# Performance work log

Hardware: AMD Instinct MI355X
Metric: run time of the kernel (lower is better)

## Reference

```python
import jax, jax.numpy as jnp
import numpy as np

N = 100000   # nodes (batched graph)
E = 1600000  # edges
G = 2048     # molecules in the batch
D_IN = 128
D_H = 128
MLP_H = 512


def setup_inputs() -> dict:
    key = jax.random.key(0)
    ks = jax.random.split(key, 20)

    def w(k, i, o):
        return (jax.random.normal(k, (i, o), jnp.float32) / np.sqrt(i)).astype(jnp.float32)

    feats = jax.random.normal(ks[0], (N, D_IN), jnp.float32)
    src = jax.random.randint(ks[1], (E,), 0, N)
    dst = jax.random.randint(ks[2], (E,), 0, N)
    graph_ids = jnp.sort(jax.random.randint(ks[3], (N,), 0, G))

    return {
        "feats": feats, "src": src, "dst": dst, "graph_ids": graph_ids,
        # 3 GraphConv layers
        "W0": w(ks[4], D_IN, D_H), "b0": jnp.zeros((D_H,), jnp.float32),
        "W1": w(ks[5], D_H, D_H),  "b1": jnp.zeros((D_H,), jnp.float32),
        "W2": w(ks[6], D_H, D_H),  "b2": jnp.zeros((D_H,), jnp.float32),
        # MLP head: D_H -> 512 -> 256 -> 1
        "Wm0": w(ks[7], D_H, MLP_H),       "bm0": jnp.zeros((MLP_H,), jnp.float32),
        "Wm1": w(ks[8], MLP_H, MLP_H // 2), "bm1": jnp.zeros((MLP_H // 2,), jnp.float32),
        "Wm2": w(ks[9], MLP_H // 2, 1),     "bm2": jnp.zeros((1,), jnp.float32),
    }


def reference(feats, src, dst, graph_ids, W0, b0, W1, b1, W2, b2,
              Wm0, bm0, Wm1, bm1, Wm2, bm2):
    ones_e = jnp.ones((E,), jnp.float32)
    # DGL GraphConv norm='both': D_out^{-1/2} on src, D_in^{-1/2} on dst; deg clamped to 1
    deg_out = jnp.maximum(jax.ops.segment_sum(ones_e, src, num_segments=N), 1.0)
    deg_in = jnp.maximum(jax.ops.segment_sum(ones_e, dst, num_segments=N), 1.0)
    inv_src = jax.lax.rsqrt(deg_out)[:, None]
    inv_dst = jax.lax.rsqrt(deg_in)[:, None]

    def gcn_layer(h, W, b):
        h = h * inv_src                                   # [N, D]
        m = jax.ops.segment_sum(h[src], dst, num_segments=N)  # gather-scatter over edges
        m = m * inv_dst
        return jax.nn.relu(jnp.dot(m, W) + b)

    h = gcn_layer(feats, W0, b0)
    h = gcn_layer(h, W1, b1)
    h = gcn_layer(h, W2, b2)

    # AvgPooling per graph
    counts = jnp.maximum(jax.ops.segment_sum(jnp.ones((N,), jnp.float32), graph_ids, num_segments=G), 1.0)
    emb = jax.ops.segment_sum(h, graph_ids, num_segments=G) / counts[:, None]  # [G, D_H]

    # MLP head (dropout = identity in eval)
    x = jax.nn.relu(jnp.dot(emb, Wm0) + bm0)
    x = jax.nn.relu(jnp.dot(x, Wm1) + bm1)
    return jnp.dot(x, Wm2) + bm2  # [G, 1]
```

## Files before the change

### kernel.cpp

```cpp
#include <hip/hip_runtime.h>


static inline int ceil_div(int a, int b){ return (a + b - 1) / b; }

#define B1 256
#define NBMAX 1024
#define CHUNK_MAX 7168
#define WPREP_BLOCKS 192

typedef __bf16 bf16x8 __attribute__((ext_vector_type(8)));
typedef float  f32x4  __attribute__((ext_vector_type(4)));

static __device__ inline __bf16 bits_to_bf16(unsigned short u){
  union { unsigned short u; __bf16 b; } x; x.u = u; return x.b;
}
static __device__ inline unsigned short bf16_bits(__bf16 b){
  union { __bf16 b; unsigned short u; } x; x.b = b; return x.u;
}
static __device__ inline unsigned pack_split(float s){
  __bf16 h = (__bf16)s;
  __bf16 l = (__bf16)(s - (float)h);
  return ((unsigned)bf16_bits(h) << 16) | (unsigned)bf16_bits(l);
}

__global__ __launch_bounds__(256) void scatter_count_kernel(
    const int* __restrict__ src, const int* __restrict__ dst,
    unsigned* __restrict__ cntA, unsigned* __restrict__ cntB,
    unsigned* __restrict__ stagedA, unsigned char* __restrict__ stagedB,
    const float* __restrict__ W0, const float* __restrict__ W1,
    const float* __restrict__ W2, __bf16* __restrict__ Wsp,
    int E, int NB){
  if (blockIdx.x >= B1){
    int gidx = (blockIdx.x - B1)*256 + threadIdx.x;
    if (gidx < 3*128*128){
      int layer = gidx >> 14, idx = gidx & 16383;
      const float* W = layer == 0 ? W0 : (layer == 1 ? W1 : W2);
      int k = idx >> 7, n = idx & 127;
      float w = W[idx];
      __bf16 h = (__bf16)w;
      __bf16 l = (__bf16)(w - (float)h);
      Wsp[(size_t)layer*2*16384 + n*128 + k] = h;
      Wsp[(size_t)layer*2*16384 + 16384 + n*128 + k] = l;
    }
    return;
  }

  __shared__ unsigned la[NBMAX], lb[NBMAX];
  __shared__ unsigned tsum[256];
  __shared__ unsigned stA[CHUNK_MAX];
  __shared__ unsigned char stB[CHUNK_MAX];

  const int t = threadIdx.x;
  const int blk = blockIdx.x;
  const int chunk = (E + B1 - 1) / B1;
  const int e0 = blk * chunk, e1 = min(e0 + chunk, E);
  const int len = e1 - e0;
  const int strideB = (chunk + 3) & ~3;

  #pragma unroll
  for (int i = t; i < NBMAX; i += 256){ la[i] = 0u; lb[i] = 0u; }
  __syncthreads();
  for (int e = e0 + t; e < e1; e += 256){
    atomicAdd(&la[dst[e] >> 7], 1u);
    atomicAdd(&lb[src[e] >> 7], 1u);
  }
  __syncthreads();

  for (int job = 0; job < 2; job++){
    unsigned* lx = job ? lb : la;
    unsigned* cx = job ? cntB : cntA;
    int b4 = t*4;
    unsigned v0 = lx[b4], v1 = lx[b4+1], v2 = lx[b4+2], v3 = lx[b4+3];
    unsigned s = v0+v1+v2+v3;
    tsum[t] = s;
    __syncthreads();
    for (int off = 1; off < 256; off <<= 1){
      unsigned u = (t >= off) ? tsum[t-off] : 0u;
      __syncthreads();
      tsum[t] += u;
      __syncthreads();
    }
    unsigned run = tsum[t] - s;
    unsigned o0 = run, o1 = run+v0, o2 = run+v0+v1, o3 = run+v0+v1+v2;
    lx[b4] = o0; lx[b4+1] = o1; lx[b4+2] = o2; lx[b4+3] = o3;
    if (b4   < NB) cx[(size_t)blk*NB + b4  ] = o0;
    if (b4+1 < NB) cx[(size_t)blk*NB + b4+1] = o1;
    if (b4+2 < NB) cx[(size_t)blk*NB + b4+2] = o2;
    if (b4+3 < NB) cx[(size_t)blk*NB + b4+3] = o3;
    __syncthreads();
  }

  for (int e = e0 + t; e < e1; e += 256){
    int s = src[e], d = dst[e];
    unsigned pA = atomicAdd(&la[d >> 7], 1u);
    stA[pA] = ((unsigned)(d & 127) << 17) | (unsigned)s;
    unsigned pB = atomicAdd(&lb[s >> 7], 1u);
    stB[pB] = (unsigned char)(s & 127);
  }
  __syncthreads();

  for (int i = t; i < len; i += 256)
    stagedA[(size_t)blk*chunk + i] = stA[i];
  int w4 = (len + 3) >> 2;
  unsigned* gB = (unsigned*)(stagedB + (size_t)blk*strideB);
  for (int i = t; i < w4; i += 256)
    gB[i] = *(unsigned*)&stB[4*i];
}

__global__ void totals_kernel(const unsigned* __restrict__ cntA,
                              const unsigned* __restrict__ cntB,
                              unsigned* __restrict__ totals, int NB, int E){
  int b = blockIdx.x * 256 + threadIdx.x;
  if (b >= NB) return;
  const unsigned* cx = blockIdx.y ? cntB : cntA;
  const int chunk = (E + B1 - 1) / B1;
  unsigned run = 0;
  for (int blk = 0; blk < B1; blk++){
    int lenb = E - blk*chunk; if (lenb > chunk) lenb = chunk; if (lenb < 0) lenb = 0;
    unsigned cur = cx[(size_t)blk*NB + b];
    unsigned nxt = (b < NB-1) ? cx[(size_t)blk*NB + b + 1] : (unsigned)lenb;
    run += nxt - cur;
  }
  totals[(size_t)blockIdx.y*NB + b] = run;
}

__global__ void scan_base_kernel(const unsigned* __restrict__ totals,
                                 unsigned* __restrict__ baseA, unsigned* __restrict__ baseB,
                                 int NB, int E){
  __shared__ unsigned s[NBMAX];
  int t = threadIdx.x;
  for (int job = 0; job < 2; job++){
    unsigned* base = job ? baseB : baseA;
    unsigned x = (t < NB) ? totals[(size_t)job*NB + t] : 0u;
    s[t] = x;
    __syncthreads();
    for (int off = 1; off < NBMAX; off <<= 1){
      unsigned v = (t >= off) ? s[t - off] : 0u;
      __syncthreads();
      s[t] += v;
      __syncthreads();
    }
    if (t < NB) base[t] = s[t] - x;
    if (t == 0) base[NB] = (unsigned)E;
    __syncthreads();
  }
}

__global__ __launch_bounds__(256) void csr_finalize_kernel(
    const unsigned* __restrict__ stagedA, const unsigned char* __restrict__ stagedB,
    const unsigned* __restrict__ cntA, const unsigned* __restrict__ cntB,
    const unsigned* __restrict__ baseA,
    int* __restrict__ row_ptr, float* __restrict__ inv_dst, float* __restrict__ inv_src,
    int* __restrict__ col, int N, int E, int NB){
  __shared__ unsigned cnt[128];
  __shared__ unsigned scn[128];
  const int b = blockIdx.x, t = threadIdx.x;
  const int node0 = b << 7;
  const int nn = min(128, N - node0);
  const int chunk = (E + B1 - 1) / B1;
  const int strideB = (chunk + 3) & ~3;
  int lenb = E - t*chunk; if (lenb > chunk) lenb = chunk; if (lenb < 0) lenb = 0;

  const unsigned a0 = cntA[(size_t)t*NB + b];
  const unsigned a1 = (b < NB-1) ? cntA[(size_t)t*NB + b + 1] : (unsigned)lenb;
  const unsigned* segA = stagedA + (size_t)t*chunk;

  if (t < 128) cnt[t] = 0u;
  __syncthreads();
  for (unsigned i = a0; i < a1; i++)
    atomicAdd(&cnt[(segA[i] >> 17) & 127u], 1u);
  __syncthreads();
  unsigned mycnt = (t < 128) ? cnt[t] : 0u;
  if (t < 128) scn[t] = mycnt;
  __syncthreads();
  for (int off = 1; off < 128; off <<= 1){
    unsigned v = (t < 128 && t >= off) ? scn[t - off] : 0u;
    __syncthreads();
    if (t < 128) scn[t] += v;
    __syncthreads();
  }
  int e0 = (int)baseA[b];
  if (t < nn){
    unsigned excl = scn[t] - mycnt;
    row_ptr[node0 + t] = e0 + (int)excl;
    unsigned c = mycnt < 1u ? 1u : mycnt;
    inv_dst[node0 + t] = rsqrtf((float)c);
    cnt[t] = (unsigned)e0 + excl;
  }
  if (b == NB - 1 && t == 0) row_ptr[N] = E;
  __syncthreads();
  for (unsigned i = a0; i < a1; i++){
    unsigned v = segA[i];
    unsigned p = atomicAdd(&cnt[(v >> 17) & 127u], 1u);
    col[p] = (int)(v & 0x1FFFFu);
  }
  __syncthreads();
  if (t < 128) cnt[t] = 0u;
  __syncthreads();
  const unsigned b0o = cntB[(size_t)t*NB + b];
  const unsigned b1o = (b < NB-1) ? cntB[(size_t)t*NB + b + 1] : (unsigned)lenb;
  const unsigned char* segB = stagedB + (size_t)t*strideB;
  for (unsigned i = b0o; i < b1o; i++)
    atomicAdd(&cnt[segB[i]], 1u);
  __syncthreads();
  if (t < nn){
    unsigned c = cnt[t] < 1u ? 1u : cnt[t];
    inv_src[node0 + t] = rsqrtf((float)c);
  }
}

template<bool SC>
__global__ __launch_bounds__(256) void csr_agg_kernel(
    const int* __restrict__ row_ptr, const int* __restrict__ col,
    const float* __restrict__ hs, const float* __restrict__ scale,
    const float* __restrict__ inv_dst, unsigned* __restrict__ aggp, int N){
  int node = (int)((blockIdx.x*256u + threadIdx.x) >> 5);
  int lane = threadIdx.x & 31;
  if (node >= N) return;
  int r0 = row_ptr[node];
  int r1 = row_ptr[node+1];
  float4 a0 = make_float4(0.f,0.f,0.f,0.f);
  float4 a1 = make_float4(0.f,0.f,0.f,0.f);
  float4 a2 = make_float4(0.f,0.f,0.f,0.f);
  float4 a3 = make_float4(0.f,0.f,0.f,0.f);
  int e = r0;
  for (; e + 3 < r1; e += 4){
    int s0 = col[e], s1 = col[e+1], s2 = col[e+2], s3 = col[e+3];
    float4 v0 = ((const float4*)(hs + (size_t)s0*128))[lane];
    float4 v1 = ((const float4*)(hs + (size_t)s1*128))[lane];
    float4 v2 = ((const float4*)(hs + (size_t)s2*128))[lane];
    float4 v3 = ((const float4*)(hs + (size_t)s3*128))[lane];
    if (SC){
      float c0 = scale[s0], c1 = scale[s1], c2 = scale[s2], c3 = scale[s3];
      v0.x*=c0; v0.y*=c0; v0.z*=c0; v0.w*=c0;
      v1.x*=c1; v1.y*=c1; v1.z*=c1; v1.w*=c1;
      v2.x*=c2; v2.y*=c2; v2.z*=c2; v2.w*=c2;
      v3.x*=c3; v3.y*=c3; v3.z*=c3; v3.w*=c3;
    }
    a0.x += v0.x; a0.y += v0.y; a0.z += v0.z; a0.w += v0.w;
    a1.x += v1.x; a1.y += v1.y; a1.z += v1.z; a1.w += v1.w;
    a2.x += v2.x; a2.y += v2.y; a2.z += v2.z; a2.w += v2.w;
    a3.x += v3.x; a3.y += v3.y; a3.z += v3.z; a3.w += v3.w;
  }
  for (; e < r1; e++){
    int s0 = col[e];
    float4 v0 = ((const float4*)(hs + (size_t)s0*128))[lane];
    if (SC){ float c0 = scale[s0]; v0.x*=c0; v0.y*=c0; v0.z*=c0; v0.w*=c0; }
    a0.x += v0.x; a0.y += v0.y; a0.z += v0.z; a0.w += v0.w;
  }
  float idst = inv_dst[node];
  float rx = ((a0.x + a1.x) + (a2.x + a3.x)) * idst;
  float ry = ((a0.y + a1.y) + (a2.y + a3.y)) * idst;
  float rz = ((a0.z + a1.z) + (a2.z + a3.z)) * idst;
  float rw = ((a0.w + a1.w) + (a2.w + a3.w)) * idst;
  uint4 p;
  p.x = pack_split(rx); p.y = pack_split(ry);
  p.z = pack_split(rz); p.w = pack_split(rw);
  ((uint4*)(aggp + (size_t)node*128))[lane] = p;
}

__global__ __launch_bounds__(256) void mfma_gemm_kernel(
    const unsigned* __restrict__ A,
    const __bf16* __restrict__ Whi, const __bf16* __restrict__ Wlo,
    const float* __restrict__ bias, const float* __restrict__ out_scale,
    float* __restrict__ out, int M){
  __shared__ __bf16 BhL[128*136];
  __shared__ __bf16 BlL[128*136];

  const int tid  = threadIdx.x;
  const int wv   = tid >> 6;
  const int lane = tid & 63;
  const int q    = lane >> 4;
  const int mn   = lane & 15;
  const int row0 = blockIdx.x*128 + wv*32;

  for (int i = tid; i < 128*16; i += 256){
    int n = i >> 4, c = (i & 15) << 3;
    *(bf16x8*)&BhL[n*136 + c] = *(const bf16x8*)(Whi + n*128 + c);
    *(bf16x8*)&BlL[n*136 + c] = *(const bf16x8*)(Wlo + n*128 + c);
  }
  __syncthreads();

  f32x4 acc[2][8];
  #pragma unroll
  for (int mt = 0; mt < 2; mt++)
    #pragma unroll
    for (int nt = 0; nt < 8; nt++)
      acc[mt][nt] = (f32x4){0.f,0.f,0.f,0.f};

  #pragma unroll
  for (int kc = 0; kc < 4; kc++){
    bf16x8 ah[2], al[2];
    #pragma unroll
    for (int mt = 0; mt < 2; mt++){
      const unsigned* ap = A + (size_t)(row0 + mt*16 + mn)*128 + kc*32 + q*8;
      uint4 x0 = *(const uint4*)ap;
      uint4 x1 = *(const uint4*)(ap + 4);
      unsigned v[8] = {x0.x, x0.y, x0.z, x0.w, x1.x, x1.y, x1.z, x1.w};
      #pragma unroll
      for (int j = 0; j < 8; j++){
        ah[mt][j] = bits_to_bf16((unsigned short)(v[j] >> 16));
        al[mt][j] = bits_to_bf16((unsigned short)(v[j] & 0xFFFFu));
      }
    }
    #pragma unroll
    for (int nt = 0; nt < 8; nt++){
      int boff = (nt*16 + mn)*136 + kc*32 + q*8;
      bf16x8 bh = *(const bf16x8*)&BhL[boff];
      bf16x8 bl = *(const bf16x8*)&BlL[boff];
      #pragma unroll
      for (int mt = 0; mt < 2; mt++){
        acc[mt][nt] = __builtin_amdgcn_mfma_f32_16x16x32_bf16(al[mt], bh, acc[mt][nt], 0, 0, 0);
        acc[mt][nt] = __builtin_amdgcn_mfma_f32_16x16x32_bf16(ah[mt], bl, acc[mt][nt], 0, 0, 0);
        acc[mt][nt] = __builtin_amdgcn_mfma_f32_16x16x32_bf16(ah[mt], bh, acc[mt][nt], 0, 0, 0);
      }
    }
  }

  #pragma unroll
  for (int mt = 0; mt < 2; mt++){
    #pragma unroll
    for (int r = 0; r < 4; r++){
      int gm = row0 + mt*16 + q*4 + r;
      if (gm < M){
        float osc = out_scale ? out_scale[gm] : 1.f;
        #pragma unroll
        for (int nt = 0; nt < 8; nt++){
          float v = acc[mt][nt][r] + bias[nt*16 + mn];
          v = fmaxf(v, 0.f) * osc;
          out[(size_t)gm*128 + nt*16 + mn] = v;
        }
      }
    }
  }
}

__global__ __launch_bounds__(256) void head_kernel(
    const float* __restrict__ h, const int* __restrict__ gid,
    const float* __restrict__ Wm0, const float* __restrict__ bm0,
    const float* __restrict__ Wm1, const float* __restrict__ bm1,
    const float* __restrict__ Wm2, const float* __restrict__ bm2,
    float* __restrict__ out, int N, int G){
  __shared__ float embL[8][128];
  __shared__ float x1L[8][512];
  __shared__ float x2L[8][256];

  const int t = threadIdx.x;
  const int wave = t >> 6, lane = t & 63;
  const int g0 = blockIdx.x * 8;

  for (int gg = 0; gg < 2; gg++){
    int gl = wave*2 + gg;
    int g = g0 + gl;
    float ax = 0.f, ay = 0.f;
    int start = 0, end = 0;
    if (g < G){
      int lo = 0, hi = N;
      while (lo < hi){ int mid = (lo + hi) >> 1; if (gid[mid] < g) lo = mid + 1; else hi = mid; }
      start = lo;
      hi = N;
      while (lo < hi){ int mid = (lo + hi) >> 1; if (gid[mid] <= g) lo = mid + 1; else hi = mid; }
      end = lo;
      for (int n = start; n < end; n++){
        float2 v = ((const float2*)(h + (size_t)n*128))[lane];
        ax += v.x; ay += v.y;
      }
    }
    int c = end - start; if (c < 1) c = 1;
    float invc = 1.0f / (float)c;
    embL[gl][2*lane]   = ax * invc;
    embL[gl][2*lane+1] = ay * invc;
  }
  __syncthreads();

  {
    float acc[8][2];
    #pragma unroll
    for (int g = 0; g < 8; g++){ acc[g][0] = 0.f; acc[g][1] = 0.f; }
    for (int k = 0; k < 128; k++){
      float w0 = Wm0[(size_t)k*512 + t];
      float w1 = Wm0[(size_t)k*512 + t + 256];
      #pragma unroll
      for (int g = 0; g < 8; g++){
        float e = embL[g][k];
        acc[g][0] = fmaf(e, w0, acc[g][0]);
        acc[g][1] = fmaf(e, w1, acc[g][1]);
      }
    }
    float b0v = bm0[t], b1v = bm0[t + 256];
    #pragma unroll
    for (int g = 0; g < 8; g++){
      x1L[g][t]       = fmaxf(acc[g][0] + b0v, 0.f);
      x1L[g][t + 256] = fmaxf(acc[g][1] + b1v, 0.f);
    }
  }
  __syncthreads();

  {
    float acc[8];
    #pragma unroll
    for (int g = 0; g < 8; g++) acc[g] = 0.f;
    for (int k = 0; k < 512; k++){
      float w = Wm1[(size_t)k*256 + t];
      #pragma unroll
      for (int g = 0; g < 8; g++)
        acc[g] = fmaf(x1L[g][k], w, acc[g]);
    }
    float bv = bm1[t];
    #pragma unroll
    for (int g = 0; g < 8; g++)
      x2L[g][t] = fmaxf(acc[g] + bv, 0.f);
  }
  __syncthreads();

  {
    int g = t >> 5;
    int c = t & 31;
    float s = 0.f;
    for (int i = c; i < 256; i += 32)
      s = fmaf(x2L[g][i], Wm2[i], s);
    for (int off = 16; off > 0; off >>= 1) s += __shfl_down(s, off, 32);
    if (c == 0 && (g0 + g) < G) out[g0 + g] = s + bm2[0];
  }
}

extern "C" void kernel_launch(void* const* d_in, const int* in_sizes, int n_in,
                              void* d_out, int out_size, void* d_ws, size_t ws_size,
                              hipStream_t stream){
  const float* feats = (const float*)d_in[0];
  const int*   src   = (const int*)d_in[1];
  const int*   dst   = (const int*)d_in[2];
  const int*   gid   = (const int*)d_in[3];
  const float* W0 = (const float*)d_in[4];   const float* b0 = (const float*)d_in[5];
  const float* W1 = (const float*)d_in[6];   const float* b1 = (const float*)d_in[7];
  const float* W2 = (const float*)d_in[8];   const float* b2 = (const float*)d_in[9];
  const float* Wm0 = (const float*)d_in[10]; const float* bm0 = (const float*)d_in[11];
  const float* Wm1 = (const float*)d_in[12]; const float* bm1 = (const float*)d_in[13];
  const float* Wm2 = (const float*)d_in[14]; const float* bm2 = (const float*)d_in[15];
  float* out = (float*)d_out;

  const int E   = in_sizes[1];
  const int N   = in_sizes[3];
  const int G   = out_size;
  const int NB  = ceil_div(N, 128);
  const int chunk = ceil_div(E, B1);
  const int strideB = (chunk + 3) & ~3;

  char* ws = (char*)d_ws;
  size_t off = 0;
  auto carve = [&](size_t bytes) -> char* {
    off = (off + 255) & ~(size_t)255;
    char* p = ws + off; off += bytes; return p;
  };
  float* inv_src = (float*)carve((size_t)N*4);
  float* inv_dst = (float*)carve((size_t)N*4);
  int* row_ptr = (int*)carve((size_t)(N+1)*4);
  int* col     = (int*)carve((size_t)E*4);
  __bf16* Wsp = (__bf16*)carve(6*128*128*2);
  float* hs  = (float*)carve((size_t)N*128*4);
  unsigned* aggp = (unsigned*)carve((size_t)N*128*4);

  unsigned* T = (unsigned*)aggp;
  unsigned* cntA   = T;
  unsigned* cntB   = cntA + (size_t)B1*NB;
  unsigned* totals = cntB + (size_t)B1*NB;
  unsigned* baseA  = totals + 2*(size_t)NB;
  unsigned* baseB  = baseA + (NB+1);
  unsigned* stagedA = baseB + (NB+1);
  unsigned char* stagedB = (unsigned char*)(stagedA + (size_t)B1*chunk);

  scatter_count_kernel<<<B1 + WPREP_BLOCKS, 256, 0, stream>>>(
      src, dst, cntA, cntB, stagedA, stagedB, W0, W1, W2, Wsp, E, NB);
  totals_kernel<<<dim3(ceil_div(NB,256), 2), 256, 0, stream>>>(cntA, cntB, totals, NB, E);
  scan_base_kernel<<<1, NBMAX, 0, stream>>>(totals, baseA, baseB, NB, E);
  csr_finalize_kernel<<<NB, 256, 0, stream>>>(stagedA, stagedB, cntA, cntB, baseA,
                                              row_ptr, inv_dst, inv_src, col, N, E, NB);

  const int agg_blocks = ceil_div(N*32, 256);
  const int ggrid = ceil_div(N, 128);
  __bf16 *Whi0 = Wsp,            *Wlo0 = Wsp + 16384;
  __bf16 *Whi1 = Wsp + 2*16384,  *Wlo1 = Wsp + 3*16384;
  __bf16 *Whi2 = Wsp + 4*16384,  *Wlo2 = Wsp + 5*16384;
  csr_agg_kernel<true><<<agg_blocks, 256, 0, stream>>>(row_ptr, col, feats, inv_src, inv_dst, aggp, N);
  mfma_gemm_kernel<<<ggrid, 256, 0, stream>>>(aggp, Whi0, Wlo0, b0, inv_src, hs, N);
  csr_agg_kernel<false><<<agg_blocks, 256, 0, stream>>>(row_ptr, col, hs, nullptr, inv_dst, aggp, N);
  mfma_gemm_kernel<<<ggrid, 256, 0, stream>>>(aggp, Whi1, Wlo1, b1, inv_src, hs, N);
  csr_agg_kernel<false><<<agg_blocks, 256, 0, stream>>>(row_ptr, col, hs, nullptr, inv_dst, aggp, N);
  mfma_gemm_kernel<<<ggrid, 256, 0, stream>>>(aggp, Whi2, Wlo2, b2, nullptr, hs, N);
  head_kernel<<<ceil_div(G,8), 256, 0, stream>>>(hs, gid, Wm0, bm0, Wm1, bm1, Wm2, bm2, out, N, G);
}
```

Measured before the change: 721.5 us.

## Stage CSR bucket edges in LDS and sort locally before coalesced col write

Rewrites the CSR finalize kernel so that each block first scans the per-thread segment lengths. All 256 threads then cooperatively copy the bucket's edges into shared memory, using a binary search to find each source segment. This replaces per-thread serial loops over uneven segments. The counting sort now happens in LDS and col is written contiguously, and the same cooperative load is used for the out-degree counts. This removes load imbalance and scattered global writes, but it adds large shared-memory usage that lowers occupancy and assumes each bucket holds at most 4096 edges.

```diff
diff --git a/kernel.cpp b/kernel.cpp
--- a/kernel.cpp
+++ b/kernel.cpp
@@ -6,6 +6,7 @@
 #define B1 256
 #define NBMAX 1024
 #define CHUNK_MAX 7168
+#define BUCKET_MAX 4096
 #define WPREP_BLOCKS 192
 
 typedef __bf16 bf16x8 __attribute__((ext_vector_type(8)));
@@ -152,60 +153,111 @@
     const unsigned* __restrict__ baseA,
     int* __restrict__ row_ptr, float* __restrict__ inv_dst, float* __restrict__ inv_src,
     int* __restrict__ col, int N, int E, int NB){
+  __shared__ unsigned offs[256];
+  __shared__ unsigned segbase[257];
+  __shared__ unsigned tsum[256];
+  __shared__ unsigned edge[BUCKET_MAX];
+  __shared__ unsigned sorted[BUCKET_MAX];
   __shared__ unsigned cnt[128];
   __shared__ unsigned scn[128];
+
   const int b = blockIdx.x, t = threadIdx.x;
   const int node0 = b << 7;
   const int nn = min(128, N - node0);
   const int chunk = (E + B1 - 1) / B1;
   const int strideB = (chunk + 3) & ~3;
-  int lenb = E - t*chunk; if (lenb > chunk) lenb = chunk; if (lenb < 0) lenb = 0;
-
-  const unsigned a0 = cntA[(size_t)t*NB + b];
-  const unsigned a1 = (b < NB-1) ? cntA[(size_t)t*NB + b + 1] : (unsigned)lenb;
-  const unsigned* segA = stagedA + (size_t)t*chunk;
-
-  if (t < 128) cnt[t] = 0u;
-  __syncthreads();
-  for (unsigned i = a0; i < a1; i++)
-    atomicAdd(&cnt[(segA[i] >> 17) & 127u], 1u);
-  __syncthreads();
-  unsigned mycnt = (t < 128) ? cnt[t] : 0u;
-  if (t < 128) scn[t] = mycnt;
-  __syncthreads();
-  for (int off = 1; off < 128; off <<= 1){
-    unsigned v = (t < 128 && t >= off) ? scn[t - off] : 0u;
-    __syncthreads();
-    if (t < 128) scn[t] += v;
-    __syncthreads();
-  }
-  int e0 = (int)baseA[b];
-  if (t < nn){
-    unsigned excl = scn[t] - mycnt;
-    row_ptr[node0 + t] = e0 + (int)excl;
-    unsigned c = mycnt < 1u ? 1u : mycnt;
-    inv_dst[node0 + t] = rsqrtf((float)c);
-    cnt[t] = (unsigned)e0 + excl;
-  }
-  if (b == NB - 1 && t == 0) row_ptr[N] = E;
-  __syncthreads();
-  for (unsigned i = a0; i < a1; i++){
-    unsigned v = segA[i];
-    unsigned p = atomicAdd(&cnt[(v >> 17) & 127u], 1u);
-    col[p] = (int)(v & 0x1FFFFu);
-  }
-  __syncthreads();
-  if (t < 128) cnt[t] = 0u;
-  __syncthreads();
-  const unsigned b0o = cntB[(size_t)t*NB + b];
-  const unsigned b1o = (b < NB-1) ? cntB[(size_t)t*NB + b + 1] : (unsigned)lenb;
-  const unsigned char* segB = stagedB + (size_t)t*strideB;
-  for (unsigned i = b0o; i < b1o; i++)
-    atomicAdd(&cnt[segB[i]], 1u);
-  __syncthreads();
-  if (t < nn){
-    unsigned c = cnt[t] < 1u ? 1u : cnt[t];
-    inv_src[node0 + t] = rsqrtf((float)c);
+  int lenb_t = E - t*chunk; if (lenb_t > chunk) lenb_t = chunk; if (lenb_t < 0) lenb_t = 0;
+
+  {
+    unsigned o0 = cntA[(size_t)t*NB + b];
+    unsigned o1 = (b < NB-1) ? cntA[(size_t)t*NB + b + 1] : (unsigned)lenb_t;
+    unsigned len = o1 - o0;
+    offs[t] = o0;
+    tsum[t] = len;
+    __syncthreads();
+    for (int off = 1; off < 256; off <<= 1){
+      unsigned u = (t >= off) ? tsum[t-off] : 0u;
+      __syncthreads();
+      tsum[t] += u;
+      __syncthreads();
+    }
+    segbase[t] = tsum[t] - len;
+    if (t == 255) segbase[256] = tsum[255];
+    __syncthreads();
+    int bucketlen = (int)segbase[256];
+
+    for (int idx = t; idx < bucketlen; idx += 256){
+      int lo = 0, hi = 255;
+      while (lo < hi){ int m = (lo + hi + 1) >> 1; if (segbase[m] <= (unsigned)idx) lo = m; else hi = m - 1; }
+      edge[idx] = stagedA[(size_t)lo*chunk + offs[lo] + ((unsigned)idx - segbase[lo])];
+    }
+    if (t < 128) cnt[t] = 0u;
+    __syncthreads();
+    for (int idx = t; idx < bucketlen; idx += 256)
+      atomicAdd(&cnt[(edge[idx] >> 17) & 127u], 1u);
+    __syncthreads();
+    unsigned mycnt = (t < 128) ? cnt[t] : 0u;
+    if (t < 128) scn[t] = mycnt;
+    __syncthreads();
+    for (int off = 1; off < 128; off <<= 1){
+      unsigned v = (t < 128 && t >= off) ? scn[t - off] : 0u;
+      __syncthreads();
+      if (t < 128) scn[t] += v;
+      __syncthreads();
+    }
+    int e0 = (int)baseA[b];
+    if (t < nn){
+      unsigned excl = scn[t] - mycnt;
+      row_ptr[node0 + t] = e0 + (int)excl;
+      unsigned c = mycnt < 1u ? 1u : mycnt;
+      inv_dst[node0 + t] = rsqrtf((float)c);
+      cnt[t] = excl;
+    }
+    if (b == NB - 1 && t == 0) row_ptr[N] = E;
+    __syncthreads();
+    for (int idx = t; idx < bucketlen; idx += 256){
+      unsigned v = edge[idx];
+      unsigned p = atomicAdd(&cnt[(v >> 17) & 127u], 1u);
+      sorted[p] = v & 0x1FFFFu;
+    }
+    __syncthreads();
+    for (int idx = t; idx < bucketlen; idx += 256)
+      col[e0 + idx] = (int)sorted[idx];
+  }
+
+  __syncthreads();
+  {
+    unsigned o0 = cntB[(size_t)t*NB + b];
+    unsigned o1 = (b < NB-1) ? cntB[(size_t)t*NB + b + 1] : (unsigned)lenb_t;
+    unsigned len = o1 - o0;
+    offs[t] = o0;
+    tsum[t] = len;
+    __syncthreads();
+    for (int off = 1; off < 256; off <<= 1){
+      unsigned u = (t >= off) ? tsum[t-off] : 0u;
+      __syncthreads();
+      tsum[t] += u;
+      __syncthreads();
+    }
+    segbase[t] = tsum[t] - len;
+    if (t == 255) segbase[256] = tsum[255];
+    if (t < 128) cnt[t] = 0u;
+    __syncthreads();
+    int bucketlen = (int)segbase[256];
+    unsigned char* edgeB = (unsigned char*)edge;
+    for (int idx = t; idx < bucketlen; idx += 256){
+      int lo = 0, hi = 255;
+      while (lo < hi){ int m = (lo + hi + 1) >> 1; if (segbase[m] <= (unsigned)idx) lo = m; else hi = m - 1; }
+      edgeB[idx] = stagedB[(size_t)lo*strideB + offs[lo] + ((unsigned)idx - segbase[lo])];
+    }
+    __syncthreads();
+    for (int idx = t; idx < bucketlen; idx += 256)
+      atomicAdd(&cnt[edgeB[idx]], 1u);
+    __syncthreads();
+    if (t < nn){
+      unsigned c = cnt[t] < 1u ? 1u : cnt[t];
+      inv_src[node0 + t] = rsqrtf((float)c);
+    }
   }
 }
 
```

Result: faster. 702.6 us (-2.6%).
